# Performance work log

Hardware: AMD Instinct MI355X
Metric: run time of the kernel (lower is better)

The kernel has to match this reference:

```python
import jax, jax.numpy as jnp
import numpy as np

NEG_SLOPE = 0.2  # PyG GATConv default


def _segment_softmax(logits, seg, num_segments):
    # numerically stable softmax over edges grouped by destination node
    m = jax.ops.segment_max(logits, seg, num_segments=num_segments)
    e = jnp.exp(logits - m[seg])
    s = jax.ops.segment_sum(e, seg, num_segments=num_segments)
    return e / (s[seg] + 1e-16)


def _gat_conv(x, src, dst, W, a_src, a_dst, b):
    # PyG GATConv, heads=1: h = xW; alpha_e = softmax_dst(LeakyReLU(a_s.h_src + a_d.h_dst));
    # out_i = sum_{e: dst(e)=i} alpha_e * h_src(e) + b
    N = x.shape[0]
    h = x @ W                              # [N, F_out]
    s = h @ a_src                          # [N]
    d = h @ a_dst                          # [N]
    logits = jax.nn.leaky_relu(s[src] + d[dst], NEG_SLOPE)  # [E]
    alpha = _segment_softmax(logits, dst, N)                # [E]
    msgs = h[src] * alpha[:, None]                          # [E, F_out]
    out = jax.ops.segment_sum(msgs, dst, num_segments=N)    # [N, F_out]
    return out + b


def _add_self_loops(edge_index, num_nodes):
    loops = jnp.arange(num_nodes, dtype=edge_index.dtype)
    return (jnp.concatenate([edge_index[0], loops]),
            jnp.concatenate([edge_index[1], loops]))


def setup_inputs() -> dict:
    key = jax.random.key(0)
    ks = jax.random.split(key, 10)
    N, C, H, K, E = 100000, 256, 128, 64, 1600000
    edge_index = jax.random.randint(ks[0], (2, E), 0, N, dtype=jnp.int32)
    embed = jax.random.normal(ks[1], (N, C), dtype=jnp.float32)
    W1 = jax.random.normal(ks[2], (C, H), dtype=jnp.float32) / np.sqrt(C)
    a_src1 = jax.random.normal(ks[3], (H,), dtype=jnp.float32) / np.sqrt(H)
    a_dst1 = jax.random.normal(ks[4], (H,), dtype=jnp.float32) / np.sqrt(H)
    b1 = jnp.zeros((H,), dtype=jnp.float32)
    W2 = jax.random.normal(ks[5], (H, K), dtype=jnp.float32) / np.sqrt(H)
    a_src2 = jax.random.normal(ks[6], (K,), dtype=jnp.float32) / np.sqrt(K)
    a_dst2 = jax.random.normal(ks[7], (K,), dtype=jnp.float32) / np.sqrt(K)
    b2 = jnp.zeros((K,), dtype=jnp.float32)
    return {"edge_index": edge_index, "embed": embed,
            "W1": W1, "a_src1": a_src1, "a_dst1": a_dst1, "b1": b1,
            "W2": W2, "a_src2": a_src2, "a_dst2": a_dst2, "b2": b2}


def reference(edge_index, embed, W1, a_src1, a_dst1, b1, W2, a_src2, a_dst2, b2):
    N = embed.shape[0]
    src, dst = _add_self_loops(edge_index, N)  # PyG GATConv adds self-loops by default
    x = _gat_conv(embed, src, dst, W1, a_src1, a_dst1, b1)
    x = jax.nn.relu(x)
    # F.dropout without training=... is identity at inference time
    x = _gat_conv(x, src, dst, W2, a_src2, a_dst2, b2)
    return jax.nn.sigmoid(x)
```

## Files before the change

### kernel.cpp

```cpp
#include <hip/hip_runtime.h>
#include <cmath>

static constexpr float NEG_SLOPE = 0.2f;
static constexpr int CHUNK = 6144;
static constexpr int NB1MAX = 112;
static constexpr int CAP1 = 20480;
static constexpr int SEG = 8;
static constexpr int LCAP2 = 512;
static constexpr int CAP2 = 1664;

typedef __attribute__((ext_vector_type(8))) short short8;
typedef __attribute__((ext_vector_type(4))) float f32x4;

__device__ __forceinline__ short f2bf(float f) {
  unsigned u = __float_as_uint(f);
  unsigned r = (u + 0x7FFFu + ((u >> 16) & 1u)) >> 16;
  return (short)r;
}
__device__ __forceinline__ float bf2f(short v) {
  return __uint_as_float(((unsigned)(unsigned short)v) << 16);
}

__global__ void transpose_cvt(const float* __restrict__ W, short* __restrict__ Wt,
                              int K, int C) {
  int idx = blockIdx.x * blockDim.x + threadIdx.x;
  if (idx >= K * C) return;
  int k = idx / C, c = idx % C;
  Wt[c * K + k] = f2bf(W[idx]);
}

template<int BN, int KTOT, bool A_BF16>
__launch_bounds__(256)
__global__ void gemm_mfma(const void* __restrict__ Av, const short* __restrict__ Bt,
                          const float* __restrict__ a_s, const float* __restrict__ a_d,
                          short* __restrict__ h, float* __restrict__ s,
                          float* __restrict__ d, int M) {
  constexpr int BM = 64, BK = 64;
  constexpr int NFRAG = BN / 16;
  __shared__ char smem[8192 + BN * 128];
  char* As = smem;
  char* Bs = smem + 8192;

  const int tid = threadIdx.x;
  const int row0 = blockIdx.x * BM;
  const int lane = tid & 63;
  const int w = tid >> 6;
  const int r15 = lane & 15, g = lane >> 4;

  f32x4 acc[NFRAG];
  #pragma unroll
  for (int j = 0; j < NFRAG; ++j) acc[j] = (f32x4)(0.f);

  for (int k0 = 0; k0 < KTOT; k0 += BK) {
    {
      int row = tid >> 2, q = tid & 3;
      int gr = row0 + row;
      short8 s0, s1;
      if (A_BF16) {
        const short* A = (const short*)Av;
        if (gr < M) {
          const short* ap = A + (size_t)gr * KTOT + k0 + q * 16;
          s0 = *reinterpret_cast<const short8*>(ap);
          s1 = *reinterpret_cast<const short8*>(ap + 8);
        } else {
          #pragma unroll
          for (int t = 0; t < 8; ++t) { s0[t] = 0; s1[t] = 0; }
        }
      } else {
        const float* A = (const float*)Av;
        float vv[16];
        if (gr < M) {
          const float* ap = A + (size_t)gr * KTOT + k0 + q * 16;
          #pragma unroll
          for (int t = 0; t < 4; ++t) {
            float4 v = *reinterpret_cast<const float4*>(ap + 4 * t);
            vv[4*t] = v.x; vv[4*t+1] = v.y; vv[4*t+2] = v.z; vv[4*t+3] = v.w;
          }
        } else {
          #pragma unroll
          for (int t = 0; t < 16; ++t) vv[t] = 0.f;
        }
        #pragma unroll
        for (int t = 0; t < 8; ++t) { s0[t] = f2bf(vv[t]); s1[t] = f2bf(vv[8+t]); }
      }
      int swz = (row & 7) << 4;
      int b0 = row * 128 + q * 32;
      *reinterpret_cast<short8*>(As + (b0 ^ swz)) = s0;
      *reinterpret_cast<short8*>(As + ((b0 + 16) ^ swz)) = s1;
    }
    if (BN == 128) {
      int col = tid >> 1, half = tid & 1;
      const short* bp = Bt + (size_t)col * KTOT + k0 + half * 32;
      int swz = (col & 7) << 4;
      int b0 = col * 128 + half * 64;
      #pragma unroll
      for (int t = 0; t < 4; ++t) {
        short8 v = *reinterpret_cast<const short8*>(bp + 8 * t);
        *reinterpret_cast<short8*>(Bs + ((b0 + 16 * t) ^ swz)) = v;
      }
    } else {
      int col = tid >> 2, q = tid & 3;
      const short* bp = Bt + (size_t)col * KTOT + k0 + q * 16;
      int swz = (col & 7) << 4;
      int b0 = col * 128 + q * 32;
      #pragma unroll
      for (int t = 0; t < 2; ++t) {
        short8 v = *reinterpret_cast<const short8*>(bp + 8 * t);
        *reinterpret_cast<short8*>(Bs + ((b0 + 16 * t) ^ swz)) = v;
      }
    }
    __syncthreads();
    #pragma unroll
    for (int kc = 0; kc < BK; kc += 32) {
      int arow = w * 16 + r15;
      short8 af = *reinterpret_cast<const short8*>(
          As + ((arow * 128 + (kc + g * 8) * 2) ^ ((r15 & 7) << 4)));
      #pragma unroll
      for (int j = 0; j < NFRAG; ++j) {
        int col = j * 16 + r15;
        short8 bf = *reinterpret_cast<const short8*>(
            Bs + ((col * 128 + (kc + g * 8) * 2) ^ ((r15 & 7) << 4)));
        acc[j] = __builtin_amdgcn_mfma_f32_16x16x32_bf16(af, bf, acc[j], 0, 0, 0);
      }
    }
    __syncthreads();
  }

  float ps[4] = {0.f, 0.f, 0.f, 0.f}, pd[4] = {0.f, 0.f, 0.f, 0.f};
  #pragma unroll
  for (int j = 0; j < NFRAG; ++j) {
    float asj = a_s[j * 16 + r15], adj = a_d[j * 16 + r15];
    #pragma unroll
    for (int r = 0; r < 4; ++r) {
      ps[r] = fmaf(acc[j][r], asj, ps[r]);
      pd[r] = fmaf(acc[j][r], adj, pd[r]);
    }
  }
  #pragma unroll
  for (int off = 1; off < 16; off <<= 1) {
    #pragma unroll
    for (int r = 0; r < 4; ++r) {
      ps[r] += __shfl_xor(ps[r], off);
      pd[r] += __shfl_xor(pd[r], off);
    }
  }
  #pragma unroll
  for (int r = 0; r < 4; ++r) {
    int gr = row0 + w * 16 + g * 4 + r;
    if (gr < M) {
      #pragma unroll
      for (int j = 0; j < NFRAG; ++j)
        h[(size_t)gr * BN + j * 16 + r15] = f2bf(acc[j][r]);
      if (r15 == 0) { s[gr] = ps[r]; d[gr] = pd[r]; }
    }
  }
}

__global__ void split1(const int* __restrict__ ei, int E, int Et, int NB1,
                       int* __restrict__ cnt1, unsigned* __restrict__ rec1) {
  __shared__ int lcnt[NB1MAX];
  __shared__ int base[NB1MAX];
  int tid = threadIdx.x;
  for (int i = tid; i < NB1; i += 256) lcnt[i] = 0;
  __syncthreads();
  int e0 = blockIdx.x * CHUNK;
  int e1 = min(e0 + CHUNK, Et);
  for (int e = e0 + tid; e < e1; e += 256) {
    int di = (e < E) ? ei[E + e] : (e - E);
    atomicAdd(&lcnt[di >> 10], 1);
  }
  __syncthreads();
  for (int i = tid; i < NB1; i += 256) {
    base[i] = atomicAdd(&cnt1[i], lcnt[i]);
    lcnt[i] = 0;
  }
  __syncthreads();
  for (int e = e0 + tid; e < e1; e += 256) {
    int si, di;
    if (e < E) { si = ei[e]; di = ei[E + e]; }
    else       { si = e - E; di = si; }
    int g = di >> 10;
    unsigned r = ((unsigned)si << 10) | (unsigned)(di & 1023);
    int p = atomicAdd(&lcnt[g], 1);
    __builtin_nontemporal_store(r, rec1 + (size_t)g * CAP1 + base[g] + p);
  }
}

__global__ void split2(const unsigned* __restrict__ rec1, const int* __restrict__ cnt1,
                       int* __restrict__ cnt2, unsigned* __restrict__ rec2) {
  __shared__ unsigned bins[16 * LCAP2];
  __shared__ int lcnt[16], base[16];
  int g1 = blockIdx.x / SEG, seg = blockIdx.x % SEG;
  int cnt = cnt1[g1];
  int len = (cnt + SEG - 1) / SEG;
  int lo = seg * len, hi = min(lo + len, cnt);
  int tid = threadIdx.x;
  if (tid < 16) lcnt[tid] = 0;
  __syncthreads();
  for (int i = lo + tid; i < hi; i += 256) {
    unsigned r = __builtin_nontemporal_load(rec1 + (size_t)g1 * CAP1 + i);
    int dloc = (int)(r & 1023u);
    int f = dloc >> 6;
    unsigned r2 = ((r >> 10) << 6) | (unsigned)(dloc & 63);
    int p = atomicAdd(&lcnt[f], 1);
    if (p < LCAP2) bins[f * LCAP2 + p] = r2;
    else {
      int gp = atomicAdd(&cnt2[g1 * 16 + f], 1);
      rec2[(size_t)(g1 * 16 + f) * CAP2 + gp] = r2;
    }
  }
  __syncthreads();
  if (tid < 16) {
    int c = min(lcnt[tid], LCAP2);
    lcnt[tid] = c;
    base[tid] = atomicAdd(&cnt2[g1 * 16 + tid], c);
  }
  __syncthreads();
  for (int f = 0; f < 16; ++f) {
    int c = lcnt[f], bs = base[f];
    for (int t = tid; t < c; t += 256)
      rec2[(size_t)(g1 * 16 + f) * CAP2 + bs + t] = bins[f * LCAP2 + t];
  }
}

__global__ void scan_bins(const int* __restrict__ cnt2, int* __restrict__ binbase,
                          int NB2, int Et, int* __restrict__ row_ptr, int N) {
  __shared__ int part[256];
  __shared__ int vals[2048];
  int tid = threadIdx.x;
  int b0 = tid * 8;
  int lsum = 0;
  #pragma unroll
  for (int k = 0; k < 8; ++k) {
    int i = b0 + k;
    int v = (i < NB2) ? cnt2[i] : 0;
    vals[i] = lsum;
    lsum += v;
  }
  part[tid] = lsum;
  __syncthreads();
  for (int off = 1; off < 256; off <<= 1) {
    int t = (tid >= off) ? part[tid - off] : 0;
    __syncthreads();
    part[tid] += t;
    __syncthreads();
  }
  int pbase = part[tid] - lsum;
  #pragma unroll
  for (int k = 0; k < 8; ++k) {
    int i = b0 + k;
    if (i < NB2) binbase[i] = pbase + vals[i];
  }
  if (tid == 0) row_ptr[N] = Et;
}

__global__ void binsort(const unsigned* __restrict__ rec2, const int* __restrict__ cnt2,
                        const int* __restrict__ binbase, int* __restrict__ row_ptr,
                        int* __restrict__ col, int N) {
  __shared__ int cur[64];
  int bid = blockIdx.x;
  int dst0 = bid << 6;
  int cnt = cnt2[bid], base = binbase[bid];
  int tid = threadIdx.x;
  if (tid < 64) cur[tid] = 0;
  __syncthreads();
  const unsigned* rp = rec2 + (size_t)bid * CAP2;
  for (int i = tid; i < cnt; i += 256) atomicAdd(&cur[rp[i] & 63u], 1);
  __syncthreads();
  if (tid < 64) {
    int v = cur[tid];
    int x = v;
    #pragma unroll
    for (int off = 1; off < 64; off <<= 1) {
      int t = __shfl_up(x, off);
      if (tid >= off) x += t;
    }
    int excl = x - v;
    cur[tid] = excl;
    if (dst0 + tid < N) row_ptr[dst0 + tid] = base + excl;
  }
  __syncthreads();
  for (int i = tid; i < cnt; i += 256) {
    unsigned r = rp[i];
    int dl = (int)(r & 63u);
    int p = atomicAdd(&cur[dl], 1);
    col[base + p] = (int)(r >> 6);
  }
}

template<int F, int ACT, bool OUT_BF16>
__global__ void gat_aggregate(const int* __restrict__ row_ptr, const int* __restrict__ col,
                              const float* __restrict__ s, const float* __restrict__ d,
                              const short* __restrict__ hb, const float* __restrict__ b,
                              void* __restrict__ out, int N) {
  constexpr int GL = F / 8;
  constexpr int NG = 64 / GL;
  int wv = (blockIdx.x * blockDim.x + threadIdx.x) >> 6;
  int lane = threadIdx.x & 63;
  if (wv >= N) return;
  const int start = row_ptr[wv];
  const int end   = row_ptr[wv + 1];
  const float dd = d[wv];
  const int gl = lane % GL;
  const int g  = lane / GL;

  float acc[8];
  #pragma unroll
  for (int t = 0; t < 8; ++t) acc[t] = 0.f;
  float wsum = 0.f;

  for (int c0 = start; c0 < end; c0 += 64) {
    int j = c0 + lane;
    int li = (j < end) ? col[j] : 0;
    float w = 0.f;
    if (j < end) {
      float l = s[li] + dd;
      l = (l > 0.f) ? l : NEG_SLOPE * l;
      w = __expf(l);
    }
    wsum += w;
    int nn = min(64, end - c0);
    for (int kk = 0; kk < nn; kk += NG) {
      int e = kk + g;
      float we = __shfl(w, e);
      int   se = __shfl(li, e);
      if (e < nn) {
        short8 v = *reinterpret_cast<const short8*>(hb + (size_t)se * F + gl * 8);
        #pragma unroll
        for (int t = 0; t < 8; ++t) acc[t] = fmaf(we, bf2f(v[t]), acc[t]);
      }
    }
  }
  #pragma unroll
  for (int off = 32; off; off >>= 1) wsum += __shfl_xor(wsum, off);
  #pragma unroll
  for (int off = GL; off < 64; off <<= 1) {
    #pragma unroll
    for (int t = 0; t < 8; ++t) acc[t] += __shfl_xor(acc[t], off);
  }
  float inv = 1.f / (wsum + 1e-16f);

  if (F == 128) {
    int c = gl * 8 + g * 2;
    float o0 = fmaf(acc[g*2],     inv, b[c]);
    float o1 = fmaf(acc[g*2 + 1], inv, b[c + 1]);
    if (ACT == 0) { o0 = fmaxf(o0, 0.f); o1 = fmaxf(o1, 0.f); }
    else { o0 = 1.f / (1.f + __expf(-o0)); o1 = 1.f / (1.f + __expf(-o1)); }
    if (OUT_BF16) {
      unsigned p = ((unsigned)(unsigned short)f2bf(o1) << 16) | (unsigned short)f2bf(o0);
      reinterpret_cast<unsigned*>(out)[((size_t)wv * F + c) >> 1] = p;
    } else {
      reinterpret_cast<float2*>(out)[((size_t)wv * F + c) >> 1] = make_float2(o0, o1);
    }
  } else {
    int c = gl * 8 + g;
    float o0 = fmaf(acc[g], inv, b[c]);
    if (ACT == 0) o0 = fmaxf(o0, 0.f);
    else o0 = 1.f / (1.f + __expf(-o0));
    if (OUT_BF16) reinterpret_cast<short*>(out)[(size_t)wv * F + c] = f2bf(o0);
    else          reinterpret_cast<float*>(out)[(size_t)wv * F + c] = o0;
  }
}

extern "C" void kernel_launch(void* const* d_in, const int* in_sizes, int n_in,
                              void* d_out, int out_size, void* d_ws, size_t ws_size,
                              hipStream_t stream) {
  const int*   ei     = (const int*)d_in[0];
  const float* embed  = (const float*)d_in[1];
  const float* W1     = (const float*)d_in[2];
  const float* a_src1 = (const float*)d_in[3];
  const float* a_dst1 = (const float*)d_in[4];
  const float* b1     = (const float*)d_in[5];
  const float* W2     = (const float*)d_in[6];
  const float* a_src2 = (const float*)d_in[7];
  const float* a_dst2 = (const float*)d_in[8];
  const float* b2     = (const float*)d_in[9];

  const int E  = in_sizes[0] / 2;
  const int H  = in_sizes[3];
  const int C  = in_sizes[2] / H;
  const int N  = in_sizes[1] / C;
  const int Et = E + N;
  const int NB1 = (N + 1023) >> 10;
  const int NB2 = NB1 << 4;

  auto al16 = [](size_t x) { return (x + 15) & ~(size_t)15; };
  char* p = (char*)d_ws;
  short* hb = (short*)p;         p += al16((size_t)N * 128 * 2);
  short* xb = (short*)p;         p += al16((size_t)N * 128 * 2);
  float* sv = (float*)p;         p += al16((size_t)N * 4);
  float* dv = (float*)p;         p += al16((size_t)N * 4);
  int* row_ptr = (int*)p;        p += al16((size_t)(N + 1) * 4);
  int* col = (int*)p;            p += al16((size_t)Et * 4);
  int* cnt1 = (int*)p;
  int* cnt2 = cnt1 + NB1;        p += al16((size_t)(NB1 + NB2) * 4);
  int* binbase = (int*)p;        p += al16((size_t)NB2 * 4);
  unsigned* rec1 = (unsigned*)p; p += al16((size_t)NB1 * CAP1 * 4);
  unsigned* rec2 = (unsigned*)p; p += al16((size_t)NB2 * CAP2 * 4);
  short* Wt1 = (short*)p;        p += al16((size_t)C * H * 2);
  short* Wt2 = (short*)p;

  dim3 blk(256);

  transpose_cvt<<<dim3((C*H + 255)/256), blk, 0, stream>>>(W1, Wt1, C, H);
  transpose_cvt<<<dim3((H*64 + 255)/256), blk, 0, stream>>>(W2, Wt2, H, 64);

  hipMemsetAsync(cnt1, 0, (size_t)(NB1 + NB2) * sizeof(int), stream);
  split1<<<dim3((Et + CHUNK - 1)/CHUNK), blk, 0, stream>>>(ei, E, Et, NB1, cnt1, rec1);
  split2<<<dim3(NB1 * SEG), blk, 0, stream>>>(rec1, cnt1, cnt2, rec2);
  scan_bins<<<dim3(1), blk, 0, stream>>>(cnt2, binbase, NB2, Et, row_ptr, N);
  binsort<<<dim3(NB2), blk, 0, stream>>>(rec2, cnt2, binbase, row_ptr, col, N);

  gemm_mfma<128, 256, false><<<dim3((N + 63)/64), blk, 0, stream>>>(embed, Wt1, a_src1,
                                                                    a_dst1, hb, sv, dv, N);
  gat_aggregate<128,0,true><<<dim3((N + 3)/4), blk, 0, stream>>>(row_ptr, col, sv, dv,
                                                                 hb, b1, xb, N);

  gemm_mfma<64, 128, true><<<dim3((N + 63)/64), blk, 0, stream>>>(xb, Wt2, a_src2,
                                                                  a_dst2, hb, sv, dv, N);
  gat_aggregate<64,1,false><<<dim3((N + 3)/4), blk, 0, stream>>>(row_ptr, col, sv, dv,
                                                                 hb, b2, d_out, N);
}
```

Before: 252.6 us.

## Fuse edge split pass with layer-1 GEMM and vectorize aggregate FMAs

The first edge-bucketing pass and the layer-1 MFMA GEMM become one launch: the first NS blocks do the split work and the remaining blocks do GEMM tiles, so the two independent jobs run concurrently and one launch is removed. Separately, the aggregation inner loop unpacks bf16 pairs with shift/mask and uses packed two-wide FMAs, with the node row offset precomputed before the shuffle. The fused kernel carries the larger GEMM shared-memory footprint for split blocks too, and its branch may raise register pressure.

```diff
diff --git a/kernel.cpp b/kernel.cpp
--- a/kernel.cpp
+++ b/kernel.cpp
@@ -11,14 +11,12 @@
 
 typedef __attribute__((ext_vector_type(8))) short short8;
 typedef __attribute__((ext_vector_type(4))) float f32x4;
+typedef __attribute__((ext_vector_type(2))) float f32x2;
 
 __device__ __forceinline__ short f2bf(float f) {
   unsigned u = __float_as_uint(f);
   unsigned r = (u + 0x7FFFu + ((u >> 16) & 1u)) >> 16;
   return (short)r;
-}
-__device__ __forceinline__ float bf2f(short v) {
-  return __uint_as_float(((unsigned)(unsigned short)v) << 16);
 }
 
 __global__ void transpose_cvt(const float* __restrict__ W, short* __restrict__ Wt,
@@ -30,19 +28,18 @@
 }
 
 template<int BN, int KTOT, bool A_BF16>
-__launch_bounds__(256)
-__global__ void gemm_mfma(const void* __restrict__ Av, const short* __restrict__ Bt,
-                          const float* __restrict__ a_s, const float* __restrict__ a_d,
-                          short* __restrict__ h, float* __restrict__ s,
-                          float* __restrict__ d, int M) {
+__device__ __forceinline__
+void gemm_body(int bid, const void* __restrict__ Av, const short* __restrict__ Bt,
+               const float* __restrict__ a_s, const float* __restrict__ a_d,
+               short* __restrict__ h, float* __restrict__ s,
+               float* __restrict__ d, int M, char* smem) {
   constexpr int BM = 64, BK = 64;
   constexpr int NFRAG = BN / 16;
-  __shared__ char smem[8192 + BN * 128];
   char* As = smem;
   char* Bs = smem + 8192;
 
   const int tid = threadIdx.x;
-  const int row0 = blockIdx.x * BM;
+  const int row0 = bid * BM;
   const int lane = tid & 63;
   const int w = tid >> 6;
   const int r15 = lane & 15, g = lane >> 4;
@@ -156,14 +153,15 @@
   }
 }
 
-__global__ void split1(const int* __restrict__ ei, int E, int Et, int NB1,
-                       int* __restrict__ cnt1, unsigned* __restrict__ rec1) {
-  __shared__ int lcnt[NB1MAX];
-  __shared__ int base[NB1MAX];
+__device__ __forceinline__
+void split1_body(int bid, const int* __restrict__ ei, int E, int Et, int NB1,
+                 int* __restrict__ cnt1, unsigned* __restrict__ rec1, char* smem) {
+  int* lcnt = (int*)smem;
+  int* base = lcnt + NB1MAX;
   int tid = threadIdx.x;
   for (int i = tid; i < NB1; i += 256) lcnt[i] = 0;
   __syncthreads();
-  int e0 = blockIdx.x * CHUNK;
+  int e0 = bid * CHUNK;
   int e1 = min(e0 + CHUNK, Et);
   for (int e = e0 + tid; e < e1; e += 256) {
     int di = (e < E) ? ei[E + e] : (e - E);
@@ -184,6 +182,33 @@
     int p = atomicAdd(&lcnt[g], 1);
     __builtin_nontemporal_store(r, rec1 + (size_t)g * CAP1 + base[g] + p);
   }
+}
+
+template<int BN, int KTOT, bool A_BF16>
+__launch_bounds__(256)
+__global__ void fused_split_gemm(const int* __restrict__ ei, int E, int Et, int NB1,
+                                 int* __restrict__ cnt1, unsigned* __restrict__ rec1,
+                                 int NS, const void* __restrict__ Av,
+                                 const short* __restrict__ Bt,
+                                 const float* __restrict__ a_s,
+                                 const float* __restrict__ a_d,
+                                 short* __restrict__ h, float* __restrict__ s,
+                                 float* __restrict__ d, int M) {
+  __shared__ char smem[8192 + BN * 128];
+  if ((int)blockIdx.x < NS)
+    split1_body(blockIdx.x, ei, E, Et, NB1, cnt1, rec1, smem);
+  else
+    gemm_body<BN, KTOT, A_BF16>(blockIdx.x - NS, Av, Bt, a_s, a_d, h, s, d, M, smem);
+}
+
+template<int BN, int KTOT, bool A_BF16>
+__launch_bounds__(256)
+__global__ void gemm_mfma(const void* __restrict__ Av, const short* __restrict__ Bt,
+                          const float* __restrict__ a_s, const float* __restrict__ a_d,
+                          short* __restrict__ h, float* __restrict__ s,
+                          float* __restrict__ d, int M) {
+  __shared__ char smem[8192 + BN * 128];
+  gemm_body<BN, KTOT, A_BF16>(blockIdx.x, Av, Bt, a_s, a_d, h, s, d, M, smem);
 }
 
 __global__ void split2(const unsigned* __restrict__ rec1, const int* __restrict__ cnt1,
@@ -303,10 +328,11 @@
   const float dd = d[wv];
   const int gl = lane % GL;
   const int g  = lane / GL;
-
-  float acc[8];
-  #pragma unroll
-  for (int t = 0; t < 8; ++t) acc[t] = 0.f;
+  const short* hbase = hb + gl * 8;
+
+  f32x2 acc2[4];
+  #pragma unroll
+  for (int t = 0; t < 4; ++t) { acc2[t][0] = 0.f; acc2[t][1] = 0.f; }
   float wsum = 0.f;
 
   for (int c0 = start; c0 < end; c0 += 64) {
@@ -319,15 +345,24 @@
       w = __expf(l);
     }
     wsum += w;
+    int off = li * F;
     int nn = min(64, end - c0);
     for (int kk = 0; kk < nn; kk += NG) {
       int e = kk + g;
       float we = __shfl(w, e);
-      int   se = __shfl(li, e);
+      int   oe = __shfl(off, e);
       if (e < nn) {
-        short8 v = *reinterpret_cast<const short8*>(hb + (size_t)se * F + gl * 8);
-        #pragma unroll
-        for (int t = 0; t < 8; ++t) acc[t] = fmaf(we, bf2f(v[t]), acc[t]);
+        uint4 v = *reinterpret_cast<const uint4*>(hbase + oe);
+        f32x2 wv2; wv2[0] = we; wv2[1] = we;
+        f32x2 p0, p1, p2, p3;
+        p0[0] = __uint_as_float(v.x << 16); p0[1] = __uint_as_float(v.x & 0xFFFF0000u);
+        p1[0] = __uint_as_float(v.y << 16); p1[1] = __uint_as_float(v.y & 0xFFFF0000u);
+        p2[0] = __uint_as_float(v.z << 16); p2[1] = __uint_as_float(v.z & 0xFFFF0000u);
+        p3[0] = __uint_as_float(v.w << 16); p3[1] = __uint_as_float(v.w & 0xFFFF0000u);
+        acc2[0] = __builtin_elementwise_fma(wv2, p0, acc2[0]);
+        acc2[1] = __builtin_elementwise_fma(wv2, p1, acc2[1]);
+        acc2[2] = __builtin_elementwise_fma(wv2, p2, acc2[2]);
+        acc2[3] = __builtin_elementwise_fma(wv2, p3, acc2[3]);
       }
     }
   }
@@ -336,14 +371,17 @@
   #pragma unroll
   for (int off = GL; off < 64; off <<= 1) {
     #pragma unroll
-    for (int t = 0; t < 8; ++t) acc[t] += __shfl_xor(acc[t], off);
+    for (int t = 0; t < 4; ++t) {
+      acc2[t][0] += __shfl_xor(acc2[t][0], off);
+      acc2[t][1] += __shfl_xor(acc2[t][1], off);
+    }
   }
   float inv = 1.f / (wsum + 1e-16f);
 
   if (F == 128) {
     int c = gl * 8 + g * 2;
-    float o0 = fmaf(acc[g*2],     inv, b[c]);
-    float o1 = fmaf(acc[g*2 + 1], inv, b[c + 1]);
+    float o0 = fmaf(acc2[g][0], inv, b[c]);
+    float o1 = fmaf(acc2[g][1], inv, b[c + 1]);
     if (ACT == 0) { o0 = fmaxf(o0, 0.f); o1 = fmaxf(o1, 0.f); }
     else { o0 = 1.f / (1.f + __expf(-o0)); o1 = 1.f / (1.f + __expf(-o1)); }
     if (OUT_BF16) {
@@ -354,7 +392,8 @@
     }
   } else {
     int c = gl * 8 + g;
-    float o0 = fmaf(acc[g], inv, b[c]);
+    float av = (g & 1) ? acc2[g >> 1][1] : acc2[g >> 1][0];
+    float o0 = fmaf(av, inv, b[c]);
     if (ACT == 0) o0 = fmaxf(o0, 0.f);
     else o0 = 1.f / (1.f + __expf(-o0));
     if (OUT_BF16) reinterpret_cast<short*>(out)[(size_t)wv * F + c] = f2bf(o0);
@@ -383,6 +422,7 @@
   const int Et = E + N;
   const int NB1 = (N + 1023) >> 10;
   const int NB2 = NB1 << 4;
+  const int NS  = (Et + CHUNK - 1) / CHUNK;
 
   auto al16 = [](size_t x) { return (x + 15) & ~(size_t)15; };
   char* p = (char*)d_ws;
@@ -404,15 +444,15 @@
 
   transpose_cvt<<<dim3((C*H + 255)/256), blk, 0, stream>>>(W1, Wt1, C, H);
   transpose_cvt<<<dim3((H*64 + 255)/256), blk, 0, stream>>>(W2, Wt2, H, 64);
-
   hipMemsetAsync(cnt1, 0, (size_t)(NB1 + NB2) * sizeof(int), stream);
-  split1<<<dim3((Et + CHUNK - 1)/CHUNK), blk, 0, stream>>>(ei, E, Et, NB1, cnt1, rec1);
+
+  fused_split_gemm<128, 256, false><<<dim3(NS + (N + 63)/64), blk, 0, stream>>>(
+      ei, E, Et, NB1, cnt1, rec1, NS, embed, Wt1, a_src1, a_dst1, hb, sv, dv, N);
+
   split2<<<dim3(NB1 * SEG), blk, 0, stream>>>(rec1, cnt1, cnt2, rec2);
   scan_bins<<<dim3(1), blk, 0, stream>>>(cnt2, binbase, NB2, Et, row_ptr, N);
   binsort<<<dim3(NB2), blk, 0, stream>>>(rec2, cnt2, binbase, row_ptr, col, N);
 
-  gemm_mfma<128, 256, false><<<dim3((N + 63)/64), blk, 0, stream>>>(embed, Wt1, a_src1,
-                                                                    a_dst1, hb, sv, dv, N);
   gat_aggregate<128,0,true><<<dim3((N + 3)/4), blk, 0, stream>>>(row_ptr, col, sv, dv,
                                                                  hb, b1, xb, N);
 
```

Result: faster. 234.9 us (-7.0%).
